# Kernel tuning notes

Measured on AMD Instinct MI355X. Metric: run time of the kernel, lower is better.

Reference implementation:

```python
import jax, jax.numpy as jnp
import numpy as np

N, E = 100000, 1600000
IN_DIM, HID, OUT, L = 64, 64, 10, 3
BN_EPS = 1e-5

def _bn(x, g, b):
    # BatchNorm1d training-mode forward: biased variance over the node axis
    m = jnp.mean(x, axis=0)
    v = jnp.var(x, axis=0)
    return (x - m) * jax.lax.rsqrt(v + BN_EPS) * g + b

def setup_inputs() -> dict:
    key = jax.random.key(0)
    ks = jax.random.split(key, 16)
    s_in = 1.0 / np.sqrt(IN_DIM)
    s_h = 1.0 / np.sqrt(HID)
    s_c = 1.0 / np.sqrt(HID * (L + 1))
    return {
        "x": jax.random.normal(ks[0], (N, IN_DIM), jnp.float32),
        "edge_index": jax.random.randint(ks[1], (2, E), 0, N, jnp.int32),
        "W_in": jax.random.uniform(ks[2], (IN_DIM, HID), jnp.float32, -s_in, s_in),
        "b_in": jnp.zeros((HID,), jnp.float32),
        "g_in": jnp.ones((HID,), jnp.float32),
        "be_in": jnp.zeros((HID,), jnp.float32),
        "eps": jnp.full((L,), 0.1, jnp.float32),
        "W1": jax.random.uniform(ks[3], (L, HID, HID), jnp.float32, -s_h, s_h),
        "b1": jnp.zeros((L, HID), jnp.float32),
        "g1": jnp.ones((L, HID), jnp.float32),
        "be1": jnp.zeros((L, HID), jnp.float32),
        "W2": jax.random.uniform(ks[4], (L, HID, HID), jnp.float32, -s_h, s_h),
        "b2": jnp.zeros((L, HID), jnp.float32),
        "g2": jnp.ones((L, HID), jnp.float32),
        "be2": jnp.zeros((L, HID), jnp.float32),
        "g_post": jnp.ones((L, HID), jnp.float32),
        "be_post": jnp.zeros((L, HID), jnp.float32),
        "W_out1": jax.random.uniform(ks[5], (HID * (L + 1), HID), jnp.float32, -s_c, s_c),
        "b_out1": jnp.zeros((HID,), jnp.float32),
        "g_out": jnp.ones((HID,), jnp.float32),
        "be_out": jnp.zeros((HID,), jnp.float32),
        "W_out2": jax.random.uniform(ks[6], (HID, OUT), jnp.float32, -s_h, s_h),
        "b_out2": jnp.zeros((OUT,), jnp.float32),
    }

def reference(x, edge_index, W_in, b_in, g_in, be_in, eps, W1, b1, g1, be1,
              W2, b2, g2, be2, g_post, be_post, W_out1, b_out1, g_out, be_out,
              W_out2, b_out2):
    src, dst = edge_index[0], edge_index[1]
    # input projection (dropout is identity in eval)
    h = jax.nn.relu(_bn(x @ W_in + b_in, g_in, be_in))
    layer_outputs = [h]
    for i in range(L):
        # GIN aggregation: gather neighbor feats, scatter-add to dst
        aggr = jax.ops.segment_sum(h[src], dst, num_segments=N)  # (N, HID)
        o = (1.0 + eps[i]) * h + aggr
        o = jax.nn.relu(_bn(o @ W1[i] + b1[i], g1[i], be1[i]))
        o = jax.nn.relu(_bn(o @ W2[i] + b2[i], g2[i], be2[i]))
        h = jax.nn.relu(_bn(o, g_post[i], be_post[i]))
        layer_outputs.append(h)
    h = jnp.concatenate(layer_outputs, axis=-1)  # (N, 4*HID)
    h = jax.nn.relu(_bn(h @ W_out1 + b_out1, g_out, be_out))
    return h @ W_out2 + b_out2
```

## Files before the change

kernel.cpp:

```cpp
#include <hip/hip_runtime.h>


#define HID 64
#define LAYERS 3
#define BN_EPS 1e-5f

#define BK_SHIFT 8
#define BK_MAX 512
#define PART_EPT 16

__device__ __forceinline__ float relu_aff(float x, float s, float t) {
    return fmaxf(fmaf(x, s, t), 0.f);
}

__device__ __forceinline__ void bn_fin(const float* __restrict__ raw, const float* __restrict__ g,
                                       const float* __restrict__ b, float invN, int c,
                                       float& s, float& t) {
    float m = raw[c] * invN;
    float v = fmaf(-m, m, raw[64 + c] * invN);
    float r = rsqrtf(v + BN_EPS);
    s = r * g[c];
    t = fmaf(-m, s, b[c]);
}


__global__ __launch_bounds__(256) void k_bhist(const int* __restrict__ dst, int* __restrict__ gh,
                                               int E, int nbk) {
    __shared__ int h[BK_MAX];
    for (int i = threadIdx.x; i < BK_MAX; i += 256) h[i] = 0;
    __syncthreads();
    int stride = gridDim.x * 256;
    for (int e = blockIdx.x * 256 + threadIdx.x; e < E; e += stride)
        atomicAdd(&h[dst[e] >> BK_SHIFT], 1);
    __syncthreads();
    for (int i = threadIdx.x; i < nbk; i += 256)
        if (h[i]) atomicAdd(&gh[i], h[i]);
}

__global__ __launch_bounds__(512) void k_bscan(const int* __restrict__ gh, int* __restrict__ boff,
                                               int* __restrict__ gcur, int nbk) {
    int lane = threadIdx.x & 63, wid = threadIdx.x >> 6;
    int v = (threadIdx.x < nbk) ? gh[threadIdx.x] : 0;
    int incl = v;
    for (int d = 1; d < 64; d <<= 1) { int y = __shfl_up(incl, d); if (lane >= d) incl += y; }
    __shared__ int ws[8];
    if (lane == 63) ws[wid] = incl;
    __syncthreads();
    if (threadIdx.x == 0) { int a = 0; for (int w = 0; w < 8; w++) { int t = ws[w]; ws[w] = a; a += t; } }
    __syncthreads();
    int excl = incl - v + ws[wid];
    if (threadIdx.x < nbk) { boff[threadIdx.x] = excl; gcur[threadIdx.x] = excl; }
    if (threadIdx.x == nbk - 1) boff[nbk] = excl + v;
}

__global__ __launch_bounds__(256) void k_bpart(const int* __restrict__ src, const int* __restrict__ dst,
                                               int* __restrict__ gcur, unsigned* __restrict__ pairs,
                                               int E) {
    __shared__ int h[BK_MAX], cur[BK_MAX], base[BK_MAX];
    int e0 = blockIdx.x * (256 * PART_EPT);
    int eend = min(e0 + 256 * PART_EPT, E);
    for (int i = threadIdx.x; i < BK_MAX; i += 256) h[i] = 0;
    __syncthreads();
    for (int e = e0 + threadIdx.x; e < eend; e += 256)
        atomicAdd(&h[dst[e] >> BK_SHIFT], 1);
    __syncthreads();
    for (int i = threadIdx.x; i < BK_MAX; i += 256) {
        cur[i] = 0;
        base[i] = h[i] ? atomicAdd(&gcur[i], h[i]) : 0;
    }
    __syncthreads();
    for (int e = e0 + threadIdx.x; e < eend; e += 256) {
        int d = dst[e];
        int b = d >> BK_SHIFT;
        int r = atomicAdd(&cur[b], 1);
        pairs[base[b] + r] = ((unsigned)(d & ((1 << BK_SHIFT) - 1)) << 24) | (unsigned)src[e];
    }
}

__global__ __launch_bounds__(256) void k_bucket_csr(const unsigned* __restrict__ pairs,
                                                    const int* __restrict__ boff,
                                                    int* __restrict__ row_off, int* __restrict__ col,
                                                    int N, int E, int nbk) {
    int b = blockIdx.x;
    int p0 = boff[b], p1 = boff[b + 1];
    int base_node = b << BK_SHIFT;
    int nn = min(256, N - base_node);
    __shared__ int h[256], cur[256];
    h[threadIdx.x] = 0;
    __syncthreads();
    for (int p = p0 + threadIdx.x; p < p1; p += 256)
        atomicAdd(&h[pairs[p] >> 24], 1);
    __syncthreads();
    int v = h[threadIdx.x];
    int lane = threadIdx.x & 63, wid = threadIdx.x >> 6;
    int incl = v;
    for (int d = 1; d < 64; d <<= 1) { int y = __shfl_up(incl, d); if (lane >= d) incl += y; }
    __shared__ int ws[4];
    if (lane == 63) ws[wid] = incl;
    __syncthreads();
    if (threadIdx.x == 0) { int a = 0; for (int w = 0; w < 4; w++) { int t = ws[w]; ws[w] = a; a += t; } }
    __syncthreads();
    int excl = incl - v + ws[wid];
    if (threadIdx.x < nn) row_off[base_node + threadIdx.x] = p0 + excl;
    if (b == nbk - 1 && threadIdx.x == 0) row_off[N] = E;
    cur[threadIdx.x] = excl;
    __syncthreads();
    for (int p = p0 + threadIdx.x; p < p1; p += 256) {
        unsigned pk = pairs[p];
        int local = pk >> 24;
        int r = atomicAdd(&cur[local], 1);
        col[p0 + r] = (int)(pk & 0xFFFFFFu);
    }
}

__global__ __launch_bounds__(256) void k_redstats(const float* __restrict__ pst,
                                                  float* __restrict__ rawOut, int nblk) {
    int slot = blockIdx.x * 4 + (threadIdx.x >> 6);
    int lane = threadIdx.x & 63;
    float s = 0.f;
    for (int b = lane; b < nblk; b += 64) s += pst[(size_t)b * 128 + slot];
#pragma unroll
    for (int m = 1; m < 64; m <<= 1) s += __shfl_xor(s, m, 64);
    if (lane == 0) rawOut[slot] = s;
}

#define GEMM44_COMPUTE(sAT, sW, acc, r0, c0)                                \
    _Pragma("unroll 8")                                                     \
    for (int k = 0; k < HID; k++) {                                         \
        float4 a = *(const float4*)&sAT[k * 65 + r0];                       \
        float4 w = *(const float4*)&sW[k * HID + c0];                       \
        acc[0]  = fmaf(a.x, w.x, acc[0]);  acc[1]  = fmaf(a.x, w.y, acc[1]);\
        acc[2]  = fmaf(a.x, w.z, acc[2]);  acc[3]  = fmaf(a.x, w.w, acc[3]);\
        acc[4]  = fmaf(a.y, w.x, acc[4]);  acc[5]  = fmaf(a.y, w.y, acc[5]);\
        acc[6]  = fmaf(a.y, w.z, acc[6]);  acc[7]  = fmaf(a.y, w.w, acc[7]);\
        acc[8]  = fmaf(a.z, w.x, acc[8]);  acc[9]  = fmaf(a.z, w.y, acc[9]);\
        acc[10] = fmaf(a.z, w.z, acc[10]); acc[11] = fmaf(a.z, w.w, acc[11]);\
        acc[12] = fmaf(a.w, w.x, acc[12]); acc[13] = fmaf(a.w, w.y, acc[13]);\
        acc[14] = fmaf(a.w, w.z, acc[14]); acc[15] = fmaf(a.w, w.w, acc[15]);\
    }

#define GEMM44_EPILOGUE(STATS_ON)                                            \
    {                                                                        \
        float4 bs = *(const float4*)&bias[c0];                               \
        float sc[4] = {0.f, 0.f, 0.f, 0.f}, sq[4] = {0.f, 0.f, 0.f, 0.f};    \
        _Pragma("unroll")                                                    \
        for (int ri = 0; ri < 4; ri++) {                                     \
            int row = base + r0 + ri;                                        \
            if (row < n) {                                                   \
                float4 v;                                                    \
                v.x = acc[ri * 4 + 0] + bs.x;                                \
                v.y = acc[ri * 4 + 1] + bs.y;                                \
                v.z = acc[ri * 4 + 2] + bs.z;                                \
                v.w = acc[ri * 4 + 3] + bs.w;                                \
                *(float4*)&C[(size_t)row * HID + c0] = v;                    \
                if (STATS_ON) {                                              \
                    sc[0] += v.x; sq[0] = fmaf(v.x, v.x, sq[0]);             \
                    sc[1] += v.y; sq[1] = fmaf(v.y, v.y, sq[1]);             \
                    sc[2] += v.z; sq[2] = fmaf(v.z, v.z, sq[2]);             \
                    sc[3] += v.w; sq[3] = fmaf(v.w, v.w, sq[3]);             \
                }                                                            \
            }                                                                \
        }                                                                    \
        if (STATS_ON) {                                                      \
            int lane = threadIdx.x & 63, wv = threadIdx.x >> 6;              \
            _Pragma("unroll")                                                \
            for (int j = 0; j < 4; j++) {                                    \
                sc[j] += __shfl_xor(sc[j], 16, 64); sc[j] += __shfl_xor(sc[j], 32, 64); \
                sq[j] += __shfl_xor(sq[j], 16, 64); sq[j] += __shfl_xor(sq[j], 32, 64); \
            }                                                                \
            if (lane < 16) {                                                 \
                *(float4*)&ps[wv][c0] = make_float4(sc[0], sc[1], sc[2], sc[3]); \
                *(float4*)&pq[wv][c0] = make_float4(sq[0], sq[1], sq[2], sq[3]); \
            }                                                                \
            __syncthreads();                                                 \
            if (threadIdx.x < 64) {                                          \
                float s = ps[0][threadIdx.x] + ps[1][threadIdx.x] + ps[2][threadIdx.x] + ps[3][threadIdx.x]; \
                float q = pq[0][threadIdx.x] + pq[1][threadIdx.x] + pq[2][threadIdx.x] + pq[3][threadIdx.x]; \
                pst[(size_t)blockIdx.x * 128 + threadIdx.x] = s;             \
                pst[(size_t)blockIdx.x * 128 + 64 + threadIdx.x] = q;        \
            }                                                                \
        }                                                                    \
    }

template <bool AFF, bool STATS>
__global__ __launch_bounds__(256) void k_gemm_t64(const float* __restrict__ A,
                                                  const float* __restrict__ raw, const float* __restrict__ g,
                                                  const float* __restrict__ b, float invN,
                                                  const float* __restrict__ W, const float* __restrict__ bias,
                                                  float* __restrict__ C, float* __restrict__ pst, int n) {
    __shared__ float stl[2 * HID];
    __shared__ float sAT[HID * 65];
    __shared__ float sW[HID * HID];
    __shared__ float ps[4][HID], pq[4][HID];
    if (AFF) {
        if (threadIdx.x < HID) {
            float s, t;
            bn_fin(raw, g, b, invN, threadIdx.x, s, t);
            stl[threadIdx.x] = s;
            stl[HID + threadIdx.x] = t;
        }
        __syncthreads();
    }
    int base = blockIdx.x * 64;
#pragma unroll
    for (int it = 0; it < 4; it++) {
        int idx = it * 256 + threadIdx.x;
        *(float4*)&sW[idx * 4] = *(const float4*)&W[idx * 4];
    }
#pragma unroll
    for (int it = 0; it < 4; it++) {
        int idx = it * 256 + threadIdx.x;
        int r = idx >> 4;
        int kc = (idx & 15) * 4;
        float4 v = make_float4(0.f, 0.f, 0.f, 0.f);
        if (base + r < n) {
            v = *(const float4*)&A[(size_t)(base + r) * HID + kc];
            if (AFF) {
                v.x = relu_aff(v.x, stl[kc + 0], stl[HID + kc + 0]);
                v.y = relu_aff(v.y, stl[kc + 1], stl[HID + kc + 1]);
                v.z = relu_aff(v.z, stl[kc + 2], stl[HID + kc + 2]);
                v.w = relu_aff(v.w, stl[kc + 3], stl[HID + kc + 3]);
            }
        }
        sAT[(kc + 0) * 65 + r] = v.x;
        sAT[(kc + 1) * 65 + r] = v.y;
        sAT[(kc + 2) * 65 + r] = v.z;
        sAT[(kc + 3) * 65 + r] = v.w;
    }
    __syncthreads();

    int c0 = (threadIdx.x & 15) * 4;
    int r0 = (threadIdx.x >> 4) * 4;
    float acc[16];
#pragma unroll
    for (int j = 0; j < 16; j++) acc[j] = 0.f;
    GEMM44_COMPUTE(sAT, sW, acc, r0, c0)
    GEMM44_EPILOGUE(STATS)
}

__global__ __launch_bounds__(256) void k_agg_gemm(const float* __restrict__ hb,
                                                  const float* __restrict__ rawH, const float* __restrict__ gH,
                                                  const float* __restrict__ bH, float invN,
                                                  const int* __restrict__ row_off, const int* __restrict__ col,
                                                  const float* __restrict__ epsp, int li,
                                                  const float* __restrict__ W, const float* __restrict__ bias,
                                                  float* __restrict__ C, float* __restrict__ pst, int n) {
    __shared__ float sAT[HID * 65];
    __shared__ float sW[HID * HID];
    __shared__ float ps[4][HID], pq[4][HID];

    int base = blockIdx.x * 64;
    int lane = threadIdx.x & 63, wv = threadIdx.x >> 6;
    int sub = lane >> 4;
    int fc = (lane & 15) * 4;

#pragma unroll
    for (int it = 0; it < 4; it++) {
        int idx = it * 256 + threadIdx.x;
        *(float4*)&sW[idx * 4] = *(const float4*)&W[idx * 4];
    }

    float s0, t0, s1, t1, s2, t2, s3, t3;
    bn_fin(rawH, gH, bH, invN, fc + 0, s0, t0);
    bn_fin(rawH, gH, bH, invN, fc + 1, s1, t1);
    bn_fin(rawH, gH, bH, invN, fc + 2, s2, t2);
    bn_fin(rawH, gH, bH, invN, fc + 3, s3, t3);
    float ope = 1.f + epsp[li];

    for (int ii = 0; ii < 16; ii++) {
        int r = wv * 16 + ii;
        int node = base + r;
        float ax = 0.f, ay = 0.f, az = 0.f, aw = 0.f;
        if (node < n) {
            int e = row_off[node], e1 = row_off[node + 1];
            while (e + 16 <= e1) {
                int i0 = col[e + sub], i1 = col[e + 4 + sub];
                int i2 = col[e + 8 + sub], i3 = col[e + 12 + sub];
                float4 v0 = *(const float4*)&hb[(size_t)i0 * HID + fc];
                float4 v1 = *(const float4*)&hb[(size_t)i1 * HID + fc];
                float4 v2 = *(const float4*)&hb[(size_t)i2 * HID + fc];
                float4 v3 = *(const float4*)&hb[(size_t)i3 * HID + fc];
                ax += relu_aff(v0.x, s0, t0) + relu_aff(v1.x, s0, t0) + relu_aff(v2.x, s0, t0) + relu_aff(v3.x, s0, t0);
                ay += relu_aff(v0.y, s1, t1) + relu_aff(v1.y, s1, t1) + relu_aff(v2.y, s1, t1) + relu_aff(v3.y, s1, t1);
                az += relu_aff(v0.z, s2, t2) + relu_aff(v1.z, s2, t2) + relu_aff(v2.z, s2, t2) + relu_aff(v3.z, s2, t2);
                aw += relu_aff(v0.w, s3, t3) + relu_aff(v1.w, s3, t3) + relu_aff(v2.w, s3, t3) + relu_aff(v3.w, s3, t3);
                e += 16;
            }
            while (e + 4 <= e1) {
                int i = col[e + sub];
                float4 v = *(const float4*)&hb[(size_t)i * HID + fc];
                ax += relu_aff(v.x, s0, t0);
                ay += relu_aff(v.y, s1, t1);
                az += relu_aff(v.z, s2, t2);
                aw += relu_aff(v.w, s3, t3);
                e += 4;
            }
            int rem = e1 - e;
            if (sub < rem) {
                int i = col[e + sub];
                float4 v = *(const float4*)&hb[(size_t)i * HID + fc];
                ax += relu_aff(v.x, s0, t0);
                ay += relu_aff(v.y, s1, t1);
                az += relu_aff(v.z, s2, t2);
                aw += relu_aff(v.w, s3, t3);
            }
        }
        ax += __shfl_xor(ax, 16, 64); ay += __shfl_xor(ay, 16, 64);
        az += __shfl_xor(az, 16, 64); aw += __shfl_xor(aw, 16, 64);
        ax += __shfl_xor(ax, 32, 64); ay += __shfl_xor(ay, 32, 64);
        az += __shfl_xor(az, 32, 64); aw += __shfl_xor(aw, 32, 64);
        if (sub == 0) {
            if (node < n) {
                float4 h4 = *(const float4*)&hb[(size_t)node * HID + fc];
                ax = fmaf(ope, relu_aff(h4.x, s0, t0), ax);
                ay = fmaf(ope, relu_aff(h4.y, s1, t1), ay);
                az = fmaf(ope, relu_aff(h4.z, s2, t2), az);
                aw = fmaf(ope, relu_aff(h4.w, s3, t3), aw);
            }
            sAT[(fc + 0) * 65 + r] = ax;
            sAT[(fc + 1) * 65 + r] = ay;
            sAT[(fc + 2) * 65 + r] = az;
            sAT[(fc + 3) * 65 + r] = aw;
        }
    }
    __syncthreads();

    int c0 = (threadIdx.x & 15) * 4;
    int r0 = (threadIdx.x >> 4) * 4;
    float acc[16];
#pragma unroll
    for (int j = 0; j < 16; j++) acc[j] = 0.f;
    GEMM44_COMPUTE(sAT, sW, acc, r0, c0)
    GEMM44_EPILOGUE(true)
}

__global__ __launch_bounds__(256) void k_gemm_out1_t(const float* __restrict__ B0, const float* __restrict__ B1,
                                                     const float* __restrict__ B2, const float* __restrict__ B3,
                                                     const float* __restrict__ R0, const float* __restrict__ R1,
                                                     const float* __restrict__ R2, const float* __restrict__ R3,
                                                     const float* __restrict__ G0, const float* __restrict__ G1,
                                                     const float* __restrict__ G2, const float* __restrict__ G3,
                                                     const float* __restrict__ E0, const float* __restrict__ E1,
                                                     const float* __restrict__ E2, const float* __restrict__ E3,
                                                     float invN,
                                                     const float* __restrict__ W, const float* __restrict__ bias,
                                                     float* __restrict__ C, float* __restrict__ pst, int n) {
    __shared__ float stl[4][2 * HID];
    __shared__ float sAT[HID * 65];
    __shared__ float sW[HID * HID];
    __shared__ float ps[4][HID], pq[4][HID];
    {
        int p = threadIdx.x >> 6, c = threadIdx.x & 63;
        const float* rp[4] = {R0, R1, R2, R3};
        const float* gp[4] = {G0, G1, G2, G3};
        const float* ep[4] = {E0, E1, E2, E3};
        float s, t;
        bn_fin(rp[p], gp[p], ep[p], invN, c, s, t);
        stl[p][c] = s;
        stl[p][HID + c] = t;
    }
    __syncthreads();

    int base = blockIdx.x * 64;
    int c0 = (threadIdx.x & 15) * 4;
    int r0 = (threadIdx.x >> 4) * 4;
    float acc[16];
#pragma unroll
    for (int j = 0; j < 16; j++) acc[j] = 0.f;
    const float* bufs[4] = {B0, B1, B2, B3};
#pragma unroll
    for (int pp = 0; pp < 4; pp++) {
        if (pp) __syncthreads();
        const float* Bp = bufs[pp];
        const float* Wp = W + (size_t)pp * HID * HID;
#pragma unroll
        for (int it = 0; it < 4; it++) {
            int idx = it * 256 + threadIdx.x;
            *(float4*)&sW[idx * 4] = *(const float4*)&Wp[idx * 4];
        }
#pragma unroll
        for (int it = 0; it < 4; it++) {
            int idx = it * 256 + threadIdx.x;
            int r = idx >> 4;
            int kc = (idx & 15) * 4;
            float4 v = make_float4(0.f, 0.f, 0.f, 0.f);
            if (base + r < n) {
                v = *(const float4*)&Bp[(size_t)(base + r) * HID + kc];
                v.x = relu_aff(v.x, stl[pp][kc + 0], stl[pp][HID + kc + 0]);
                v.y = relu_aff(v.y, stl[pp][kc + 1], stl[pp][HID + kc + 1]);
                v.z = relu_aff(v.z, stl[pp][kc + 2], stl[pp][HID + kc + 2]);
                v.w = relu_aff(v.w, stl[pp][kc + 3], stl[pp][HID + kc + 3]);
            }
            sAT[(kc + 0) * 65 + r] = v.x;
            sAT[(kc + 1) * 65 + r] = v.y;
            sAT[(kc + 2) * 65 + r] = v.z;
            sAT[(kc + 3) * 65 + r] = v.w;
        }
        __syncthreads();
        GEMM44_COMPUTE(sAT, sW, acc, r0, c0)
    }
    GEMM44_EPILOGUE(true)
}

__global__ __launch_bounds__(256) void k_gemm_out2_t(const float* __restrict__ A,
                                                     const float* __restrict__ raw, const float* __restrict__ g,
                                                     const float* __restrict__ b, float invN,
                                                     const float* __restrict__ W, const float* __restrict__ bias,
                                                     float* __restrict__ C, int n) {
    __shared__ float stl[2 * HID];
    if (threadIdx.x < HID) {
        float s, t;
        bn_fin(raw, g, b, invN, threadIdx.x, s, t);
        stl[threadIdx.x] = s;
        stl[HID + threadIdx.x] = t;
    }
    __syncthreads();
    int lane = threadIdx.x & 63;
    int wv = threadIdx.x >> 6;
    int k0 = __builtin_amdgcn_readfirstlane(wv * 16);
    int row = blockIdx.x * 64 + lane;
    bool valid = row < n;
    float acc[10];
#pragma unroll
    for (int j = 0; j < 10; j++) acc[j] = 0.f;
    if (valid) {
        const float4* a4 = (const float4*)(A + (size_t)row * HID + k0);
#pragma unroll
        for (int kk = 0; kk < 4; kk++) {
            float4 av = a4[kk];
            float a[4] = {av.x, av.y, av.z, av.w};
#pragma unroll
            for (int u = 0; u < 4; u++) {
                int k = k0 + kk * 4 + u;
                float xv = relu_aff(a[u], stl[k], stl[HID + k]);
#pragma unroll
                for (int j = 0; j < 10; j++) acc[j] = fmaf(xv, W[k * 10 + j], acc[j]);
            }
        }
    }
    __shared__ float part[4][64][10];
#pragma unroll
    for (int j = 0; j < 10; j++) part[wv][lane][j] = acc[j];
    __syncthreads();
    if (wv == 0 && valid) {
        float* cp = C + (size_t)row * 10;
#pragma unroll
        for (int j = 0; j < 10; j++)
            cp[j] = bias[j] + part[0][lane][j] + part[1][lane][j] + part[2][lane][j] + part[3][lane][j];
    }
}

__global__ __launch_bounds__(256) void k_affine_stats(float* __restrict__ X,
                                                      const float* __restrict__ rawIn,
                                                      const float* __restrict__ g, const float* __restrict__ b,
                                                      float invN,
                                                      float* __restrict__ pst, long long n64) {
    long long stride = (long long)gridDim.x * 256;
    long long i0 = (long long)blockIdx.x * 256 + threadIdx.x;
    int col = threadIdx.x & 63;
    float sA, tA;
    bn_fin(rawIn, g, b, invN, col, sA, tA);
    float s = 0.f, q = 0.f;
    for (long long i = i0; i < n64; i += stride) {
        float v = relu_aff(X[i], sA, tA);
        X[i] = v;
        s += v; q = fmaf(v, v, q);
    }
    __shared__ float ls[256], lq[256];
    ls[threadIdx.x] = s; lq[threadIdx.x] = q;
    __syncthreads();
    if (threadIdx.x < 64) {
        s = ls[threadIdx.x] + ls[threadIdx.x + 64] + ls[threadIdx.x + 128] + ls[threadIdx.x + 192];
        q = lq[threadIdx.x] + lq[threadIdx.x + 64] + lq[threadIdx.x + 128] + lq[threadIdx.x + 192];
        pst[(size_t)blockIdx.x * 128 + col] = s;
        pst[(size_t)blockIdx.x * 128 + 64 + col] = q;
    }
}

extern "C" void kernel_launch(void* const* d_in, const int* in_sizes, int n_in,
                              void* d_out, int out_size, void* d_ws, size_t ws_size,
                              hipStream_t stream) {
    const float* x = (const float*)d_in[0];
    const int* ei = (const int*)d_in[1];
    const float* W_in = (const float*)d_in[2];
    const float* b_in = (const float*)d_in[3];
    const float* g_in = (const float*)d_in[4];
    const float* be_in = (const float*)d_in[5];
    const float* epsp = (const float*)d_in[6];
    const float* W1 = (const float*)d_in[7];
    const float* b1 = (const float*)d_in[8];
    const float* g1 = (const float*)d_in[9];
    const float* be1 = (const float*)d_in[10];
    const float* W2 = (const float*)d_in[11];
    const float* b2 = (const float*)d_in[12];
    const float* g2 = (const float*)d_in[13];
    const float* be2 = (const float*)d_in[14];
    const float* g_post = (const float*)d_in[15];
    const float* be_post = (const float*)d_in[16];
    const float* W_out1 = (const float*)d_in[17];
    const float* b_out1 = (const float*)d_in[18];
    const float* g_out = (const float*)d_in[19];
    const float* be_out = (const float*)d_in[20];
    const float* W_out2 = (const float*)d_in[21];
    const float* b_out2 = (const float*)d_in[22];

    const int N = in_sizes[0] / HID;
    const int E = in_sizes[1] / 2;
    const int* srcp = ei;
    const int* dstp = ei + E;

    const int nbk = (N + (1 << BK_SHIFT) - 1) >> BK_SHIFT;
    if (nbk > BK_MAX) return;
    if (N > (1 << 24)) return;

    size_t NODE = (size_t)N * HID;
    float* f = (float*)d_ws;
    float* pre0 = f;
    float* z0 = f + NODE;
    float* z1 = f + 2 * NODE;
    float* z2 = f + 3 * NODE;
    float* o = f + 4 * NODE;
    float* p = f + 5 * NODE;
    int* rc = (int*)(f + 6 * NODE);
    int* col = rc + (N + 1);
    int* gh = col + E;
    int* boff = gh + 512;
    int* gcur = boff + 513;
    float* raw = (float*)(gcur + 512);
    unsigned* pairs = (unsigned*)o;

    size_t need = (size_t)(6 * NODE) * 4 + ((size_t)(N + 1) + E + 1537) * 4 + (size_t)11 * 128 * 4;
    if (ws_size < need) return;

    float invN = 1.0f / (float)N;
    int gt = (N + 63) / 64;
    int pb = (E + 256 * PART_EPT - 1) / (256 * PART_EPT);

    hipMemsetAsync(gh, 0, 512 * sizeof(int), stream);

    k_bhist<<<512, 256, 0, stream>>>(dstp, gh, E, nbk);
    k_bscan<<<1, 512, 0, stream>>>(gh, boff, gcur, nbk);
    k_bpart<<<pb, 256, 0, stream>>>(srcp, dstp, gcur, pairs, E);
    k_bucket_csr<<<nbk, 256, 0, stream>>>(pairs, boff, rc, col, N, E, nbk);

    k_gemm_t64<false, true><<<gt, 256, 0, stream>>>(x, nullptr, nullptr, nullptr, invN,
                                                    W_in, b_in, pre0, o, N);
    k_redstats<<<32, 256, 0, stream>>>(o, raw, gt);

    float* zb[3] = {z0, z1, z2};
    for (int i = 0; i < LAYERS; i++) {
        int s1 = 1 + 3 * i, s2 = 2 + 3 * i, sp = 3 + 3 * i;
        const float* hb = (i == 0) ? pre0 : zb[i - 1];
        const float* rh = (i == 0) ? raw : raw + (size_t)(3 * i) * 128;
        const float* gh2 = (i == 0) ? g_in : g_post + (i - 1) * HID;
        const float* eh = (i == 0) ? be_in : be_post + (i - 1) * HID;
        k_agg_gemm<<<gt, 256, 0, stream>>>(hb, rh, gh2, eh, invN, rc, col, epsp, i,
                                           W1 + (size_t)i * HID * HID, b1 + i * HID,
                                           p, zb[i], N);
        k_redstats<<<32, 256, 0, stream>>>(zb[i], raw + (size_t)s1 * 128, gt);
        k_gemm_t64<true, true><<<gt, 256, 0, stream>>>(p, raw + (size_t)s1 * 128, g1 + i * HID, be1 + i * HID,
                                                       invN, W2 + (size_t)i * HID * HID, b2 + i * HID,
                                                       zb[i], o, N);
        k_redstats<<<32, 256, 0, stream>>>(o, raw + (size_t)s2 * 128, gt);
        k_affine_stats<<<512, 256, 0, stream>>>(zb[i], raw + (size_t)s2 * 128, g2 + i * HID, be2 + i * HID, invN,
                                                o, (long long)NODE);
        k_redstats<<<32, 256, 0, stream>>>(o, raw + (size_t)sp * 128, 512);
    }

    k_gemm_out1_t<<<gt, 256, 0, stream>>>(pre0, z0, z1, z2,
                                          raw, raw + 3 * 128, raw + 6 * 128, raw + 9 * 128,
                                          g_in, g_post, g_post + HID, g_post + 2 * HID,
                                          be_in, be_post, be_post + HID, be_post + 2 * HID,
                                          invN, W_out1, b_out1, p, o, N);
    k_redstats<<<32, 256, 0, stream>>>(o, raw + 10 * 128, gt);
    k_gemm_out2_t<<<gt, 256, 0, stream>>>(p, raw + 10 * 128, g_out, be_out, invN,
                                          W_out2, b_out2, (float*)d_out, N);
}
```

Baseline: 796.2 us.

## Split fused aggregation+GEMM into standalone two-node-per-wave aggregation kernel

Replaces the fused aggregate-then-GEMM kernel with a separate aggregation kernel followed by the existing tiled GEMM kernel. The new aggregation kernel gives each wavefront two consecutive nodes whose CSR edge ranges are walked together with 8-way unrolled gathers, splitting the sums at the boundary, which raises memory-level parallelism and cuts per-node serial latency. The cost is an extra global write and read of the (N,64) aggregated tensor and one more launch per layer.

New measurement: 732.6 us. -8.0%, faster.

```diff
diff --git a/kernel.cpp b/kernel.cpp
--- a/kernel.cpp
+++ b/kernel.cpp
@@ -122,6 +122,116 @@
 #pragma unroll
     for (int m = 1; m < 64; m <<= 1) s += __shfl_xor(s, m, 64);
     if (lane == 0) rawOut[slot] = s;
+}
+
+
+#define AGG_ACC(V, BASE)                                                    \
+    {                                                                       \
+        float rx = relu_aff((V).x, s0, t0), ry = relu_aff((V).y, s1, t1);   \
+        float rz = relu_aff((V).z, s2, t2), rw = relu_aff((V).w, s3, t3);   \
+        aT.x += rx; aT.y += ry; aT.z += rz; aT.w += rw;                     \
+        if ((BASE) + sub < split) { aA.x += rx; aA.y += ry; aA.z += rz; aA.w += rw; } \
+    }
+
+__global__ __launch_bounds__(256) void k_agg(const float* __restrict__ hb,
+                                             const float* __restrict__ raw, const float* __restrict__ g,
+                                             const float* __restrict__ b, float invN,
+                                             const int* __restrict__ row_off, const int* __restrict__ col,
+                                             const float* __restrict__ epsp, int li,
+                                             float* __restrict__ o, int n) {
+    int wid = threadIdx.x >> 6, lane = threadIdx.x & 63;
+    int nodeA = (blockIdx.x * 4 + wid) * 2;
+    if (nodeA >= n) return;
+    int nodeB = nodeA + 1;
+    bool hasB = nodeB < n;
+    int sub = lane >> 4;
+    int fc = (lane & 15) * 4;
+    float s0, t0, s1, t1, s2, t2, s3, t3;
+    bn_fin(raw, g, b, invN, fc + 0, s0, t0);
+    bn_fin(raw, g, b, invN, fc + 1, s1, t1);
+    bn_fin(raw, g, b, invN, fc + 2, s2, t2);
+    bn_fin(raw, g, b, invN, fc + 3, s3, t3);
+
+    int e = row_off[nodeA];
+    int split = row_off[nodeA + 1];
+    int e2 = hasB ? row_off[nodeB + 1] : split;
+    float4 aT = make_float4(0.f, 0.f, 0.f, 0.f);
+    float4 aA = make_float4(0.f, 0.f, 0.f, 0.f);
+
+    while (e + 32 <= e2) {
+        int i0 = col[e + sub],      i1 = col[e + 4 + sub];
+        int i2 = col[e + 8 + sub],  i3 = col[e + 12 + sub];
+        int i4 = col[e + 16 + sub], i5 = col[e + 20 + sub];
+        int i6 = col[e + 24 + sub], i7 = col[e + 28 + sub];
+        float4 v0 = *(const float4*)&hb[(size_t)i0 * HID + fc];
+        float4 v1 = *(const float4*)&hb[(size_t)i1 * HID + fc];
+        float4 v2 = *(const float4*)&hb[(size_t)i2 * HID + fc];
+        float4 v3 = *(const float4*)&hb[(size_t)i3 * HID + fc];
+        float4 v4 = *(const float4*)&hb[(size_t)i4 * HID + fc];
+        float4 v5 = *(const float4*)&hb[(size_t)i5 * HID + fc];
+        float4 v6 = *(const float4*)&hb[(size_t)i6 * HID + fc];
+        float4 v7 = *(const float4*)&hb[(size_t)i7 * HID + fc];
+        AGG_ACC(v0, e +  0) AGG_ACC(v1, e +  4) AGG_ACC(v2, e +  8) AGG_ACC(v3, e + 12)
+        AGG_ACC(v4, e + 16) AGG_ACC(v5, e + 20) AGG_ACC(v6, e + 24) AGG_ACC(v7, e + 28)
+        e += 32;
+    }
+    if (e + 16 <= e2) {
+        int i0 = col[e + sub],     i1 = col[e + 4 + sub];
+        int i2 = col[e + 8 + sub], i3 = col[e + 12 + sub];
+        float4 v0 = *(const float4*)&hb[(size_t)i0 * HID + fc];
+        float4 v1 = *(const float4*)&hb[(size_t)i1 * HID + fc];
+        float4 v2 = *(const float4*)&hb[(size_t)i2 * HID + fc];
+        float4 v3 = *(const float4*)&hb[(size_t)i3 * HID + fc];
+        AGG_ACC(v0, e + 0) AGG_ACC(v1, e + 4) AGG_ACC(v2, e + 8) AGG_ACC(v3, e + 12)
+        e += 16;
+    }
+    if (e + 8 <= e2) {
+        int i0 = col[e + sub], i1 = col[e + 4 + sub];
+        float4 v0 = *(const float4*)&hb[(size_t)i0 * HID + fc];
+        float4 v1 = *(const float4*)&hb[(size_t)i1 * HID + fc];
+        AGG_ACC(v0, e + 0) AGG_ACC(v1, e + 4)
+        e += 8;
+    }
+    if (e + 4 <= e2) {
+        int i0 = col[e + sub];
+        float4 v0 = *(const float4*)&hb[(size_t)i0 * HID + fc];
+        AGG_ACC(v0, e)
+        e += 4;
+    }
+    int rem = e2 - e;
+    if (sub < rem) {
+        int i0 = col[e + sub];
+        float4 v0 = *(const float4*)&hb[(size_t)i0 * HID + fc];
+        AGG_ACC(v0, e)
+    }
+
+    aT.x += __shfl_xor(aT.x, 16, 64); aT.y += __shfl_xor(aT.y, 16, 64);
+    aT.z += __shfl_xor(aT.z, 16, 64); aT.w += __shfl_xor(aT.w, 16, 64);
+    aT.x += __shfl_xor(aT.x, 32, 64); aT.y += __shfl_xor(aT.y, 32, 64);
+    aT.z += __shfl_xor(aT.z, 32, 64); aT.w += __shfl_xor(aT.w, 32, 64);
+    aA.x += __shfl_xor(aA.x, 16, 64); aA.y += __shfl_xor(aA.y, 16, 64);
+    aA.z += __shfl_xor(aA.z, 16, 64); aA.w += __shfl_xor(aA.w, 16, 64);
+    aA.x += __shfl_xor(aA.x, 32, 64); aA.y += __shfl_xor(aA.y, 32, 64);
+    aA.z += __shfl_xor(aA.z, 32, 64); aA.w += __shfl_xor(aA.w, 32, 64);
+
+    float ope = 1.f + epsp[li];
+    if (sub == 0) {
+        float4 h4 = *(const float4*)&hb[(size_t)nodeA * HID + fc];
+        float4 r;
+        r.x = fmaf(ope, relu_aff(h4.x, s0, t0), aA.x);
+        r.y = fmaf(ope, relu_aff(h4.y, s1, t1), aA.y);
+        r.z = fmaf(ope, relu_aff(h4.z, s2, t2), aA.z);
+        r.w = fmaf(ope, relu_aff(h4.w, s3, t3), aA.w);
+        *(float4*)&o[(size_t)nodeA * HID + fc] = r;
+    } else if (sub == 1 && hasB) {
+        float4 h4 = *(const float4*)&hb[(size_t)nodeB * HID + fc];
+        float4 r;
+        r.x = fmaf(ope, relu_aff(h4.x, s0, t0), aT.x - aA.x);
+        r.y = fmaf(ope, relu_aff(h4.y, s1, t1), aT.y - aA.y);
+        r.z = fmaf(ope, relu_aff(h4.z, s2, t2), aT.z - aA.z);
+        r.w = fmaf(ope, relu_aff(h4.w, s3, t3), aT.w - aA.w);
+        *(float4*)&o[(size_t)nodeB * HID + fc] = r;
+    }
 }
 
 #define GEMM44_COMPUTE(sAT, sW, acc, r0, c0)                                \
@@ -238,102 +348,6 @@
     GEMM44_EPILOGUE(STATS)
 }
 
-__global__ __launch_bounds__(256) void k_agg_gemm(const float* __restrict__ hb,
-                                                  const float* __restrict__ rawH, const float* __restrict__ gH,
-                                                  const float* __restrict__ bH, float invN,
-                                                  const int* __restrict__ row_off, const int* __restrict__ col,
-                                                  const float* __restrict__ epsp, int li,
-                                                  const float* __restrict__ W, const float* __restrict__ bias,
-                                                  float* __restrict__ C, float* __restrict__ pst, int n) {
-    __shared__ float sAT[HID * 65];
-    __shared__ float sW[HID * HID];
-    __shared__ float ps[4][HID], pq[4][HID];
-
-    int base = blockIdx.x * 64;
-    int lane = threadIdx.x & 63, wv = threadIdx.x >> 6;
-    int sub = lane >> 4;
-    int fc = (lane & 15) * 4;
-
-#pragma unroll
-    for (int it = 0; it < 4; it++) {
-        int idx = it * 256 + threadIdx.x;
-        *(float4*)&sW[idx * 4] = *(const float4*)&W[idx * 4];
-    }
-
-    float s0, t0, s1, t1, s2, t2, s3, t3;
-    bn_fin(rawH, gH, bH, invN, fc + 0, s0, t0);
-    bn_fin(rawH, gH, bH, invN, fc + 1, s1, t1);
-    bn_fin(rawH, gH, bH, invN, fc + 2, s2, t2);
-    bn_fin(rawH, gH, bH, invN, fc + 3, s3, t3);
-    float ope = 1.f + epsp[li];
-
-    for (int ii = 0; ii < 16; ii++) {
-        int r = wv * 16 + ii;
-        int node = base + r;
-        float ax = 0.f, ay = 0.f, az = 0.f, aw = 0.f;
-        if (node < n) {
-            int e = row_off[node], e1 = row_off[node + 1];
-            while (e + 16 <= e1) {
-                int i0 = col[e + sub], i1 = col[e + 4 + sub];
-                int i2 = col[e + 8 + sub], i3 = col[e + 12 + sub];
-                float4 v0 = *(const float4*)&hb[(size_t)i0 * HID + fc];
-                float4 v1 = *(const float4*)&hb[(size_t)i1 * HID + fc];
-                float4 v2 = *(const float4*)&hb[(size_t)i2 * HID + fc];
-                float4 v3 = *(const float4*)&hb[(size_t)i3 * HID + fc];
-                ax += relu_aff(v0.x, s0, t0) + relu_aff(v1.x, s0, t0) + relu_aff(v2.x, s0, t0) + relu_aff(v3.x, s0, t0);
-                ay += relu_aff(v0.y, s1, t1) + relu_aff(v1.y, s1, t1) + relu_aff(v2.y, s1, t1) + relu_aff(v3.y, s1, t1);
-                az += relu_aff(v0.z, s2, t2) + relu_aff(v1.z, s2, t2) + relu_aff(v2.z, s2, t2) + relu_aff(v3.z, s2, t2);
-                aw += relu_aff(v0.w, s3, t3) + relu_aff(v1.w, s3, t3) + relu_aff(v2.w, s3, t3) + relu_aff(v3.w, s3, t3);
-                e += 16;
-            }
-            while (e + 4 <= e1) {
-                int i = col[e + sub];
-                float4 v = *(const float4*)&hb[(size_t)i * HID + fc];
-                ax += relu_aff(v.x, s0, t0);
-                ay += relu_aff(v.y, s1, t1);
-                az += relu_aff(v.z, s2, t2);
-                aw += relu_aff(v.w, s3, t3);
-                e += 4;
-            }
-            int rem = e1 - e;
-            if (sub < rem) {
-                int i = col[e + sub];
-                float4 v = *(const float4*)&hb[(size_t)i * HID + fc];
-                ax += relu_aff(v.x, s0, t0);
-                ay += relu_aff(v.y, s1, t1);
-                az += relu_aff(v.z, s2, t2);
-                aw += relu_aff(v.w, s3, t3);
-            }
-        }
-        ax += __shfl_xor(ax, 16, 64); ay += __shfl_xor(ay, 16, 64);
-        az += __shfl_xor(az, 16, 64); aw += __shfl_xor(aw, 16, 64);
-        ax += __shfl_xor(ax, 32, 64); ay += __shfl_xor(ay, 32, 64);
-        az += __shfl_xor(az, 32, 64); aw += __shfl_xor(aw, 32, 64);
-        if (sub == 0) {
-            if (node < n) {
-                float4 h4 = *(const float4*)&hb[(size_t)node * HID + fc];
-                ax = fmaf(ope, relu_aff(h4.x, s0, t0), ax);
-                ay = fmaf(ope, relu_aff(h4.y, s1, t1), ay);
-                az = fmaf(ope, relu_aff(h4.z, s2, t2), az);
-                aw = fmaf(ope, relu_aff(h4.w, s3, t3), aw);
-            }
-            sAT[(fc + 0) * 65 + r] = ax;
-            sAT[(fc + 1) * 65 + r] = ay;
-            sAT[(fc + 2) * 65 + r] = az;
-            sAT[(fc + 3) * 65 + r] = aw;
-        }
-    }
-    __syncthreads();
-
-    int c0 = (threadIdx.x & 15) * 4;
-    int r0 = (threadIdx.x >> 4) * 4;
-    float acc[16];
-#pragma unroll
-    for (int j = 0; j < 16; j++) acc[j] = 0.f;
-    GEMM44_COMPUTE(sAT, sW, acc, r0, c0)
-    GEMM44_EPILOGUE(true)
-}
-
 __global__ __launch_bounds__(256) void k_gemm_out1_t(const float* __restrict__ B0, const float* __restrict__ B1,
                                                      const float* __restrict__ B2, const float* __restrict__ B3,
                                                      const float* __restrict__ R0, const float* __restrict__ R1,
@@ -534,6 +548,7 @@
 
     float invN = 1.0f / (float)N;
     int gt = (N + 63) / 64;
+    int ga = (N + 7) / 8;
     int pb = (E + 256 * PART_EPT - 1) / (256 * PART_EPT);
 
     hipMemsetAsync(gh, 0, 512 * sizeof(int), stream);
@@ -554,9 +569,10 @@
         const float* rh = (i == 0) ? raw : raw + (size_t)(3 * i) * 128;
         const float* gh2 = (i == 0) ? g_in : g_post + (i - 1) * HID;
         const float* eh = (i == 0) ? be_in : be_post + (i - 1) * HID;
-        k_agg_gemm<<<gt, 256, 0, stream>>>(hb, rh, gh2, eh, invN, rc, col, epsp, i,
-                                           W1 + (size_t)i * HID * HID, b1 + i * HID,
-                                           p, zb[i], N);
+        k_agg<<<ga, 256, 0, stream>>>(hb, rh, gh2, eh, invN, rc, col, epsp, i, o, N);
+        k_gemm_t64<false, true><<<gt, 256, 0, stream>>>(o, nullptr, nullptr, nullptr, invN,
+                                                        W1 + (size_t)i * HID * HID, b1 + i * HID,
+                                                        p, zb[i], N);
         k_redstats<<<32, 256, 0, stream>>>(zb[i], raw + (size_t)s1 * 128, gt);
         k_gemm_t64<true, true><<<gt, 256, 0, stream>>>(p, raw + (size_t)s1 * 128, g1 + i * HID, be1 + i * HID,
                                                        invN, W2 + (size_t)i * HID * HID, b2 + i * HID,
```
